# Kernel optimization log

Measured on AMD Instinct MI355X. Metric: run time of the kernel, lower is better.

The kernel has to match this reference:

```python
import jax, jax.numpy as jnp
import numpy as np

N_NODES = 120000  # n_entities + n_users
N_REL = 16
D = 64   # entity_dim
R = 64   # relation_dim
E = 1600000


def setup_inputs() -> dict:
    key = jax.random.key(0)
    k1, k2, k3, k4, k5, k6 = jax.random.split(key, 6)
    return {
        "entity_user_embed": jax.random.normal(k1, (N_NODES, D), dtype=jnp.float32) * 0.1,
        "relation_embed": jax.random.normal(k2, (N_REL, R), dtype=jnp.float32) * 0.1,
        "W_R": jax.random.normal(k3, (N_REL, D, R), dtype=jnp.float32) * 0.1,
        "edge_src": jax.random.randint(k4, (E,), 0, N_NODES, dtype=jnp.int32),
        "edge_dst": jax.random.randint(k5, (E,), 0, N_NODES, dtype=jnp.int32),
        "edge_type": jax.random.randint(k6, (E,), 0, N_REL, dtype=jnp.int32),
    }


def reference(entity_user_embed, relation_embed, W_R, edge_src, edge_dst, edge_type):
    n_nodes = entity_user_embed.shape[0]
    # Per-relation transform of every node embedding: [n_rel, n_nodes, R].
    # Equivalent to the per-relation edge loop: matmul(emb[id], W_R[r]).
    trans = jnp.einsum('nd,rdk->rnk', entity_user_embed, W_R)
    r_mul_t = trans[edge_type, edge_src]   # [E, R] (edges.src path)
    r_mul_h = trans[edge_type, edge_dst]   # [E, R] (edges.dst path)
    r_embed = relation_embed[edge_type]    # [E, R]
    # bmm([E,1,R], [E,R,1]) -> per-edge dot product
    att = jnp.sum(r_mul_t * jnp.tanh(r_mul_h + r_embed), axis=-1)  # [E]
    # edge softmax over incoming edges of each destination node
    att_max = jax.ops.segment_max(att, edge_dst, num_segments=n_nodes)
    ex = jnp.exp(att - att_max[edge_dst])
    denom = jax.ops.segment_sum(ex, edge_dst, num_segments=n_nodes)
    out = ex / denom[edge_dst]
    return out[:, None]  # [E, 1], matching squeeze(-1) of [E,1,1]
```

## Files before the change

kernel.cpp:

```cpp
#include <hip/hip_runtime.h>
#include <hip/hip_bf16.h>

#define D64 64
#define NREL 16
#define SCALE 32.0f
#define INV_SCALE 0.03125f

typedef __attribute__((ext_vector_type(8))) short bf16x8;
typedef __attribute__((ext_vector_type(4))) float f32x4;
typedef __attribute__((ext_vector_type(2))) float f32x2;

__device__ __forceinline__ float tanh_fast(float x) {
    float e = __expf(2.0f * x);
    return 1.0f - 2.0f / (e + 1.0f);
}

__device__ __forceinline__ float tanh_poly(float x) {
    x = fmaxf(-1.5f, fminf(1.5f, x));
    float u = x * x;
    float p = fmaf(u, -0.0182227f, 0.108952f);
    p = fmaf(u, p, -0.329139f);
    p = fmaf(u, p, 1.0f);
    return x * p;
}

__device__ __forceinline__ unsigned short f2b(float x) {
    __hip_bfloat16 h = __float2bfloat16(x);
    return *reinterpret_cast<unsigned short*>(&h);
}

__global__ void zero_denom_kernel(float* __restrict__ denom, int n) {
    int i = blockIdx.x * blockDim.x + threadIdx.x;
    if (i < n) denom[i] = 0.0f;
}

__global__ void prep_kernel(const float* __restrict__ WR, const float* __restrict__ rel,
                            unsigned short* __restrict__ Wt, float* __restrict__ relp) {
    int i = blockIdx.x * blockDim.x + threadIdx.x;
    if (i < NREL * D64 * D64) {
        int r = i >> 12, rem = i & 4095, c = rem >> 6, d = rem & 63;
        Wt[i] = f2b(WR[(r << 12) + (d << 6) + c]);
    }
    if (i < NREL * D64) {
        int t = i >> 6, kp = i & 63;
        int q = kp >> 4, m = (kp >> 2) & 3, g = kp & 3;
        relp[i] = rel[t * D64 + m * 16 + q * 4 + g];
    }
}

__global__ __launch_bounds__(256)
void trans_gemm_kernel(const float* __restrict__ emb,
                       const unsigned short* __restrict__ Wt,
                       uint4* __restrict__ trans,
                       int n_nodes) {
    const int lane = threadIdx.x & 63;
    const int wid  = threadIdx.x >> 6;
    const int col  = lane & 15;
    const int quad = lane >> 4;
    const int rbase = (blockIdx.x & 1) * 8;
    const int nodebase = (blockIdx.x >> 1) * 128 + wid * 32;

    bf16x8 bfr[2][2];
    int nds[2];
    #pragma unroll
    for (int j = 0; j < 2; ++j) {
        int node = nodebase + j * 16 + col;
        nds[j] = node;
        int cn = node < n_nodes ? node : n_nodes - 1;
        const float* bp = emb + (size_t)cn * D64 + quad * 8;
        #pragma unroll
        for (int ks = 0; ks < 2; ++ks) {
            float4 v0 = *(const float4*)(bp + ks * 32);
            float4 v1 = *(const float4*)(bp + ks * 32 + 4);
            bfr[j][ks][0] = (short)f2b(v0.x); bfr[j][ks][1] = (short)f2b(v0.y);
            bfr[j][ks][2] = (short)f2b(v0.z); bfr[j][ks][3] = (short)f2b(v0.w);
            bfr[j][ks][4] = (short)f2b(v1.x); bfr[j][ks][5] = (short)f2b(v1.y);
            bfr[j][ks][6] = (short)f2b(v1.z); bfr[j][ks][7] = (short)f2b(v1.w);
        }
    }

    bf16x8 curA[4][2], nxtA[4][2];
    {
        const unsigned short* w = Wt + (rbase << 12);
        #pragma unroll
        for (int mt = 0; mt < 4; ++mt) {
            const unsigned short* ap = w + (mt * 16 + col) * D64 + quad * 8;
            curA[mt][0] = *(const bf16x8*)ap;
            curA[mt][1] = *(const bf16x8*)(ap + 32);
        }
    }

    #pragma unroll 1
    for (int rr = 0; rr < 8; ++rr) {
        const int r = rbase + rr;
        if (rr < 7) {
            const unsigned short* wn = Wt + ((r + 1) << 12);
            #pragma unroll
            for (int mt = 0; mt < 4; ++mt) {
                const unsigned short* ap = wn + (mt * 16 + col) * D64 + quad * 8;
                nxtA[mt][0] = *(const bf16x8*)ap;
                nxtA[mt][1] = *(const bf16x8*)(ap + 32);
            }
        }

        f32x4 acc[4][2];
        #pragma unroll
        for (int mt = 0; mt < 4; ++mt) {
            #pragma unroll
            for (int j = 0; j < 2; ++j) {
                f32x4 c = {0.f, 0.f, 0.f, 0.f};
                c = __builtin_amdgcn_mfma_f32_16x16x32_bf16(curA[mt][0], bfr[j][0], c, 0, 0, 0);
                c = __builtin_amdgcn_mfma_f32_16x16x32_bf16(curA[mt][1], bfr[j][1], c, 0, 0, 0);
                acc[mt][j] = c;
            }
        }
        #pragma unroll
        for (int j = 0; j < 2; ++j) {
            if (nds[j] < n_nodes) {
                uint4 pk;
                unsigned p;
                p = __builtin_amdgcn_cvt_pk_fp8_f32(acc[0][j][0] * SCALE, acc[0][j][1] * SCALE, 0, false);
                p = __builtin_amdgcn_cvt_pk_fp8_f32(acc[0][j][2] * SCALE, acc[0][j][3] * SCALE, p, true);
                pk.x = p;
                p = __builtin_amdgcn_cvt_pk_fp8_f32(acc[1][j][0] * SCALE, acc[1][j][1] * SCALE, 0, false);
                p = __builtin_amdgcn_cvt_pk_fp8_f32(acc[1][j][2] * SCALE, acc[1][j][3] * SCALE, p, true);
                pk.y = p;
                p = __builtin_amdgcn_cvt_pk_fp8_f32(acc[2][j][0] * SCALE, acc[2][j][1] * SCALE, 0, false);
                p = __builtin_amdgcn_cvt_pk_fp8_f32(acc[2][j][2] * SCALE, acc[2][j][3] * SCALE, p, true);
                pk.z = p;
                p = __builtin_amdgcn_cvt_pk_fp8_f32(acc[3][j][0] * SCALE, acc[3][j][1] * SCALE, 0, false);
                p = __builtin_amdgcn_cvt_pk_fp8_f32(acc[3][j][2] * SCALE, acc[3][j][3] * SCALE, p, true);
                pk.w = p;
                trans[((size_t)r * n_nodes + nds[j]) * 4 + quad] = pk;
            }
        }
        if (rr < 7) {
            #pragma unroll
            for (int mt = 0; mt < 4; ++mt) {
                curA[mt][0] = nxtA[mt][0];
                curA[mt][1] = nxtA[mt][1];
            }
        }
    }
}

__device__ __forceinline__ void term4(unsigned ut, unsigned uh, float4 r, float& acc) {
    f32x2 tlo = __builtin_amdgcn_cvt_pk_f32_fp8(ut, false);
    f32x2 thi = __builtin_amdgcn_cvt_pk_f32_fp8(ut, true);
    f32x2 hlo = __builtin_amdgcn_cvt_pk_f32_fp8(uh, false);
    f32x2 hhi = __builtin_amdgcn_cvt_pk_f32_fp8(uh, true);
    acc += tlo[0] * tanh_poly(fmaf(hlo[0], INV_SCALE, r.x));
    acc += tlo[1] * tanh_poly(fmaf(hlo[1], INV_SCALE, r.y));
    acc += thi[0] * tanh_poly(fmaf(hhi[0], INV_SCALE, r.z));
    acc += thi[1] * tanh_poly(fmaf(hhi[1], INV_SCALE, r.w));
}

__global__ __launch_bounds__(256)
void edge_kernel(const unsigned* __restrict__ trans,
                 const float* __restrict__ relp,
                 const int* __restrict__ esrc, const int* __restrict__ edst,
                 const int* __restrict__ etype,
                 float* __restrict__ out, float* __restrict__ denom,
                 int E, int n_nodes) {
    int e0 = blockIdx.x * 512 + threadIdx.x;
    int e1 = e0 + 256;
    bool v0 = e0 < E, v1 = e1 < E;
    int i0 = v0 ? e0 : 0;
    int i1 = v1 ? e1 : 0;
    int t0 = etype[i0], s0 = esrc[i0], d0 = edst[i0];
    int t1 = etype[i1], s1 = esrc[i1], d1 = edst[i1];

    const uint4* pt0 = (const uint4*)(trans + ((size_t)t0 * n_nodes + s0) * 16);
    const uint4* ph0 = (const uint4*)(trans + ((size_t)t0 * n_nodes + d0) * 16);
    const uint4* pt1 = (const uint4*)(trans + ((size_t)t1 * n_nodes + s1) * 16);
    const uint4* ph1 = (const uint4*)(trans + ((size_t)t1 * n_nodes + d1) * 16);

    uint4 T0[4], H0[4], T1[4], H1[4];
    #pragma unroll
    for (int c4 = 0; c4 < 4; ++c4) {
        T0[c4] = pt0[c4]; H0[c4] = ph0[c4];
        T1[c4] = pt1[c4]; H1[c4] = ph1[c4];
    }

    const float4* pr0 = (const float4*)(relp + t0 * D64);
    const float4* pr1 = (const float4*)(relp + t1 * D64);
    float a0 = 0.f, a1 = 0.f;
    #pragma unroll
    for (int c4 = 0; c4 < 4; ++c4) {
        term4(T0[c4].x, H0[c4].x, pr0[c4 * 4 + 0], a0);
        term4(T1[c4].x, H1[c4].x, pr1[c4 * 4 + 0], a1);
        term4(T0[c4].y, H0[c4].y, pr0[c4 * 4 + 1], a0);
        term4(T1[c4].y, H1[c4].y, pr1[c4 * 4 + 1], a1);
        term4(T0[c4].z, H0[c4].z, pr0[c4 * 4 + 2], a0);
        term4(T1[c4].z, H1[c4].z, pr1[c4 * 4 + 2], a1);
        term4(T0[c4].w, H0[c4].w, pr0[c4 * 4 + 3], a0);
        term4(T1[c4].w, H1[c4].w, pr1[c4 * 4 + 3], a1);
    }
    if (v0) {
        float ex = __expf(a0 * INV_SCALE);
        out[e0] = ex;
        atomicAdd(&denom[d0], ex);
    }
    if (v1) {
        float ex = __expf(a1 * INV_SCALE);
        out[e1] = ex;
        atomicAdd(&denom[d1], ex);
    }
}

__global__ void normalize_kernel(float* __restrict__ out,
                                 const float* __restrict__ denom,
                                 const int* __restrict__ edst, int E) {
    int e = blockIdx.x * blockDim.x + threadIdx.x;
    if (e < E) out[e] = out[e] / denom[edst[e]];
}

__global__ __launch_bounds__(256)
void edge_att_fallback(const float* __restrict__ emb, const float* __restrict__ rel,
                       const float* __restrict__ WR, const int* __restrict__ esrc,
                       const int* __restrict__ edst, const int* __restrict__ etype,
                       float* __restrict__ exbuf, float* __restrict__ denom,
                       int E, int chunkSize) {
    const int type = blockIdx.x & 15;
    const int c    = blockIdx.x >> 4;
    const int lane = threadIdx.x & 63;
    const int wid  = threadIdx.x >> 6;
    long base0 = (long)c * (long)chunkSize;
    long cend  = base0 + chunkSize;
    if (cend > E) cend = E;
    if (base0 >= cend) return;
    int per = (chunkSize + 3) >> 2;
    long wbeg = base0 + (long)wid * per;
    long wend = wbeg + per;
    if (wend > cend) wend = cend;
    if (wbeg >= wend) return;
    float w[D64];
    const float* Wt = WR + (size_t)type * D64 * D64;
    #pragma unroll
    for (int d = 0; d < D64; ++d) w[d] = Wt[d * D64 + lane];
    const float rk = rel[type * D64 + lane];
    for (long s0 = wbeg; s0 < wend; s0 += 64) {
        long e = s0 + lane;
        int ty = -1, sv = 0, dv = 0;
        if (e < wend) { ty = etype[e]; sv = esrc[e]; dv = edst[e]; }
        unsigned long long m = __ballot(ty == type);
        while (m) {
            int b = __builtin_ctzll(m);
            m &= m - 1;
            int sn = __builtin_amdgcn_readlane(sv, b);
            int dn = __builtin_amdgcn_readlane(dv, b);
            const float4* es4 = (const float4*)(emb + (size_t)sn * D64);
            const float4* ed4 = (const float4*)(emb + (size_t)dn * D64);
            float t0 = 0.f, t1 = 0.f, t2 = 0.f, t3 = 0.f;
            float h0 = 0.f, h1 = 0.f, h2 = 0.f, h3 = 0.f;
            #pragma unroll
            for (int i = 0; i < D64 / 4; ++i) {
                float4 a = es4[i]; float4 b4 = ed4[i];
                t0 = fmaf(a.x, w[4*i+0], t0); t1 = fmaf(a.y, w[4*i+1], t1);
                t2 = fmaf(a.z, w[4*i+2], t2); t3 = fmaf(a.w, w[4*i+3], t3);
                h0 = fmaf(b4.x, w[4*i+0], h0); h1 = fmaf(b4.y, w[4*i+1], h1);
                h2 = fmaf(b4.z, w[4*i+2], h2); h3 = fmaf(b4.w, w[4*i+3], h3);
            }
            float t = (t0 + t1) + (t2 + t3);
            float h = (h0 + h1) + (h2 + h3);
            float p = t * tanh_fast(h + rk);
            #pragma unroll
            for (int off = 32; off > 0; off >>= 1) p += __shfl_xor(p, off);
            if (lane == 0) {
                float ex = __expf(p);
                exbuf[s0 + b] = ex;
                atomicAdd(&denom[dn], ex);
            }
        }
    }
}

__global__ void normalize_fallback(float* __restrict__ out,
                                   const float* __restrict__ denom,
                                   const int* __restrict__ edst, int E) {
    int e = blockIdx.x * blockDim.x + threadIdx.x;
    if (e < E) out[e] = out[e] / denom[edst[e]];
}

extern "C" void kernel_launch(void* const* d_in, const int* in_sizes, int n_in,
                              void* d_out, int out_size, void* d_ws, size_t ws_size,
                              hipStream_t stream) {
    const float* emb  = (const float*)d_in[0];
    const float* rel  = (const float*)d_in[1];
    const float* WR   = (const float*)d_in[2];
    const int*   esrc = (const int*)d_in[3];
    const int*   edst = (const int*)d_in[4];
    const int*   ety  = (const int*)d_in[5];

    const int E       = in_sizes[3];
    const int n_nodes = in_sizes[0] / D64;
    float* out = (float*)d_out;

    size_t transB = (size_t)NREL * n_nodes * D64;
    size_t off_trans = 0;
    size_t off_wt    = (off_trans + transB + 255) & ~(size_t)255;
    size_t off_rel   = (off_wt + (size_t)NREL * D64 * D64 * 2 + 255) & ~(size_t)255;
    size_t off_den   = (off_rel + (size_t)NREL * D64 * 4 + 255) & ~(size_t)255;
    size_t need      = off_den + (size_t)n_nodes * sizeof(float);

    if (ws_size >= need) {
        uint4*          trans = (uint4*)((char*)d_ws + off_trans);
        unsigned short* Wt    = (unsigned short*)((char*)d_ws + off_wt);
        float*          relp  = (float*)((char*)d_ws + off_rel);
        float*          denom = (float*)((char*)d_ws + off_den);

        prep_kernel<<<(NREL * D64 * D64 + 255) / 256, 256, 0, stream>>>(WR, rel, Wt, relp);
        zero_denom_kernel<<<(n_nodes + 255) / 256, 256, 0, stream>>>(denom, n_nodes);
        trans_gemm_kernel<<<((n_nodes + 127) / 128) * 2, 256, 0, stream>>>(emb, Wt, trans, n_nodes);
        edge_kernel<<<(E + 511) / 512, 256, 0, stream>>>((const unsigned*)trans, relp,
                                                         esrc, edst, ety,
                                                         out, denom, E, n_nodes);
        normalize_kernel<<<(E + 255) / 256, 256, 0, stream>>>(out, denom, edst, E);
    } else {
        float* denom = (float*)d_ws;
        zero_denom_kernel<<<(n_nodes + 255) / 256, 256, 0, stream>>>(denom, n_nodes);
        const int NCHUNK = 256;
        int chunk = (E + NCHUNK - 1) / NCHUNK;
        edge_att_fallback<<<16 * NCHUNK, 256, 0, stream>>>(emb, rel, WR, esrc, edst, ety,
                                                           out, denom, E, chunk);
        normalize_fallback<<<(E + 255) / 256, 256, 0, stream>>>(out, denom, edst, E);
    }
}
```

Before: 281.0 us.

## Stage W_R tiles in double-buffered LDS and double nodes per wave

The trans GEMM kernel now loads each relation's bf16 weight tile cooperatively into a double-buffered shared-memory buffer, prefetching the next relation while computing the current one. Each wave now covers 64 nodes instead of 32, halving the grid. The goal is to cut redundant global weight loads per wave and amortize them over more MFMA work. In exchange it adds block-wide barriers and more accumulator registers, which could lower occupancy.

```diff
diff --git a/kernel.cpp b/kernel.cpp
--- a/kernel.cpp
+++ b/kernel.cpp
@@ -53,17 +53,27 @@
                        const unsigned short* __restrict__ Wt,
                        uint4* __restrict__ trans,
                        int n_nodes) {
-    const int lane = threadIdx.x & 63;
-    const int wid  = threadIdx.x >> 6;
+    __shared__ unsigned short lbuf[2][4096];
+    const int tid  = threadIdx.x;
+    const int lane = tid & 63;
+    const int wid  = tid >> 6;
     const int col  = lane & 15;
     const int quad = lane >> 4;
     const int rbase = (blockIdx.x & 1) * 8;
-    const int nodebase = (blockIdx.x >> 1) * 128 + wid * 32;
-
-    bf16x8 bfr[2][2];
-    int nds[2];
+    const int nodebase = (blockIdx.x >> 1) * 256 + wid * 64;
+
+    const int c0 = tid, c1 = tid + 256;
+    const int mt0 = c0 >> 7, q20 = (c0 >> 6) & 1, ln0 = c0 & 63;
+    const int so0 = ((mt0 * 16 + (ln0 & 15)) << 6) + (q20 << 5) + ((ln0 >> 4) << 3);
+    const int do0 = (mt0 << 10) + (q20 << 9) + (ln0 << 3);
+    const int mt1 = c1 >> 7, q21 = (c1 >> 6) & 1, ln1 = c1 & 63;
+    const int so1 = ((mt1 * 16 + (ln1 & 15)) << 6) + (q21 << 5) + ((ln1 >> 4) << 3);
+    const int do1 = (mt1 << 10) + (q21 << 9) + (ln1 << 3);
+
+    bf16x8 bfr[4][2];
+    int nds[4];
     #pragma unroll
-    for (int j = 0; j < 2; ++j) {
+    for (int j = 0; j < 4; ++j) {
         int node = nodebase + j * 16 + col;
         nds[j] = node;
         int cn = node < n_nodes ? node : n_nodes - 1;
@@ -79,43 +89,44 @@
         }
     }
 
-    bf16x8 curA[4][2], nxtA[4][2];
     {
         const unsigned short* w = Wt + (rbase << 12);
-        #pragma unroll
-        for (int mt = 0; mt < 4; ++mt) {
-            const unsigned short* ap = w + (mt * 16 + col) * D64 + quad * 8;
-            curA[mt][0] = *(const bf16x8*)ap;
-            curA[mt][1] = *(const bf16x8*)(ap + 32);
-        }
-    }
+        bf16x8 s0 = *(const bf16x8*)(w + so0);
+        bf16x8 s1 = *(const bf16x8*)(w + so1);
+        *(bf16x8*)(&lbuf[0][do0]) = s0;
+        *(bf16x8*)(&lbuf[0][do1]) = s1;
+    }
+    __syncthreads();
 
     #pragma unroll 1
     for (int rr = 0; rr < 8; ++rr) {
         const int r = rbase + rr;
+        const int cur = rr & 1;
+
+        bf16x8 n0, n1;
         if (rr < 7) {
             const unsigned short* wn = Wt + ((r + 1) << 12);
-            #pragma unroll
-            for (int mt = 0; mt < 4; ++mt) {
-                const unsigned short* ap = wn + (mt * 16 + col) * D64 + quad * 8;
-                nxtA[mt][0] = *(const bf16x8*)ap;
-                nxtA[mt][1] = *(const bf16x8*)(ap + 32);
-            }
-        }
-
-        f32x4 acc[4][2];
+            n0 = *(const bf16x8*)(wn + so0);
+            n1 = *(const bf16x8*)(wn + so1);
+        }
+
+        const unsigned short* lb = lbuf[cur];
+        f32x4 acc[4][4];
         #pragma unroll
         for (int mt = 0; mt < 4; ++mt) {
+            bf16x8 a0 = *(const bf16x8*)(lb + (mt << 10) + (lane << 3));
+            bf16x8 a1 = *(const bf16x8*)(lb + (mt << 10) + 512 + (lane << 3));
             #pragma unroll
-            for (int j = 0; j < 2; ++j) {
+            for (int j = 0; j < 4; ++j) {
                 f32x4 c = {0.f, 0.f, 0.f, 0.f};
-                c = __builtin_amdgcn_mfma_f32_16x16x32_bf16(curA[mt][0], bfr[j][0], c, 0, 0, 0);
-                c = __builtin_amdgcn_mfma_f32_16x16x32_bf16(curA[mt][1], bfr[j][1], c, 0, 0, 0);
+                c = __builtin_amdgcn_mfma_f32_16x16x32_bf16(a0, bfr[j][0], c, 0, 0, 0);
+                c = __builtin_amdgcn_mfma_f32_16x16x32_bf16(a1, bfr[j][1], c, 0, 0, 0);
                 acc[mt][j] = c;
             }
         }
+
         #pragma unroll
-        for (int j = 0; j < 2; ++j) {
+        for (int j = 0; j < 4; ++j) {
             if (nds[j] < n_nodes) {
                 uint4 pk;
                 unsigned p;
@@ -134,12 +145,11 @@
                 trans[((size_t)r * n_nodes + nds[j]) * 4 + quad] = pk;
             }
         }
+
         if (rr < 7) {
-            #pragma unroll
-            for (int mt = 0; mt < 4; ++mt) {
-                curA[mt][0] = nxtA[mt][0];
-                curA[mt][1] = nxtA[mt][1];
-            }
+            *(bf16x8*)(&lbuf[1 - cur][do0]) = n0;
+            *(bf16x8*)(&lbuf[1 - cur][do1]) = n1;
+            __syncthreads();
         }
     }
 }
@@ -311,7 +321,7 @@
 
         prep_kernel<<<(NREL * D64 * D64 + 255) / 256, 256, 0, stream>>>(WR, rel, Wt, relp);
         zero_denom_kernel<<<(n_nodes + 255) / 256, 256, 0, stream>>>(denom, n_nodes);
-        trans_gemm_kernel<<<((n_nodes + 127) / 128) * 2, 256, 0, stream>>>(emb, Wt, trans, n_nodes);
+        trans_gemm_kernel<<<((n_nodes + 255) / 256) * 2, 256, 0, stream>>>(emb, Wt, trans, n_nodes);
         edge_kernel<<<(E + 511) / 512, 256, 0, stream>>>((const unsigned*)trans, relp,
                                                          esrc, edst, ety,
                                                          out, denom, E, n_nodes);
```

Result: faster. 243.4 us (-13.4%).
